# Optimization experiments

Measured on AMD Instinct MI355X. Metric: run time of the kernel, lower is better.

The kernel has to match this reference:

```python
import jax, jax.numpy as jnp
import numpy as np

B, S, N_STATE, N_HEAD = 8, 4096, 1024, 16
N_FREQ = 10000.0
H_DIM = N_STATE // N_HEAD          # 64
N_ROTS = H_DIM // 2                # 32


def setup_inputs() -> dict:
    key = jax.random.key(0)
    k1, k2, k3, k4, k5 = jax.random.split(key, 5)
    x = jax.random.normal(k1, (B, S, N_STATE), dtype=jnp.float32)
    # rotation angles (module inits to zeros; small random values exercise the math)
    thetas = jax.random.normal(k2, (N_ROTS,), dtype=jnp.float32) * 0.1
    # r_pairs.long() in torch -> integer plane indices; ensure i != j
    i = jax.random.randint(k3, (N_ROTS,), 0, H_DIM)
    off = jax.random.randint(k4, (N_ROTS,), 1, H_DIM)
    j = (i + off) % H_DIM
    r_pairs = jnp.stack([i, j], axis=-1).astype(jnp.int32)
    theta_scale = jnp.ones((1,), dtype=jnp.float32)
    # r_matrix inits to identity; add small noise so it is non-trivial
    r_matrix = jnp.eye(H_DIM, dtype=jnp.float32) + 0.01 * jax.random.normal(k5, (H_DIM, H_DIM), dtype=jnp.float32)
    inv_freq = 1.0 / (N_FREQ ** (jnp.arange(0, H_DIM, 2, dtype=jnp.float32) / H_DIM))
    return {"x": x, "thetas": thetas, "theta_scale": theta_scale,
            "r_matrix": r_matrix, "inv_freq": inv_freq,
            "r_pairs": r_pairs, "n_head": N_HEAD}


def reference(x, thetas, theta_scale, r_matrix, inv_freq, r_pairs, n_head):
    b, s, n_state = x.shape
    h_dim = n_state // n_head
    x2d = x.reshape(-1, h_dim)  # [B*S*H, h_dim]
    angles = thetas * theta_scale[0]

    # Sequential Givens plane rotations: x @ G(i,j,theta) only touches columns i, j.
    def step(carry, inp):
        theta, ij = inp
        i, j = ij[0], ij[1]
        c, sn = jnp.cos(theta), jnp.sin(theta)
        xi = carry[:, i]
        xj = carry[:, j]
        carry = carry.at[:, i].set(xi * c + xj * sn)
        carry = carry.at[:, j].set(-xi * sn + xj * c)
        return carry, None

    x2d, _ = jax.lax.scan(step, x2d, (angles, r_pairs))
    x2d = x2d @ r_matrix
    xh = x2d.reshape(b, s, n_head, h_dim)

    # RoPE-style sin/cos mix
    pos = jnp.arange(s, dtype=jnp.float32)
    sinu = pos[:, None] * inv_freq[None, :]          # [s, h_dim//2]
    sin = jnp.sin(sinu)[None, :, None, :]
    cos = jnp.cos(sinu)[None, :, None, :]
    x1, x2 = xh[..., ::2], xh[..., 1::2]
    out = jnp.concatenate([x1 * cos - x2 * sin, x1 * sin + x2 * cos], axis=-1)
    return out.reshape(b, s, n_state)
```

## Files before the change

### kernel.cpp

```cpp
#include <hip/hip_runtime.h>
#include <cstdint>
#include <cstddef>

#define S_LEN   4096
#define NROT    32
#define NGRP    8192

typedef __attribute__((ext_vector_type(8))) short  short8x;
typedef __attribute__((ext_vector_type(4))) float  floatx4;

typedef __attribute__((address_space(1))) unsigned int gu32;
typedef __attribute__((address_space(3))) unsigned int lu32;

__device__ __host__ inline unsigned short f2bf(float f) {
  union { float f; unsigned u; } c; c.f = f;
  unsigned u = c.u;
  return (unsigned short)((u + 0x7fffu + ((u >> 16) & 1u)) >> 16);
}
__device__ inline float bf2f(unsigned short h) {
  union { unsigned u; float f; } c; c.u = ((unsigned)h) << 16;
  return c.f;
}

__global__ void setup_kernel(const float* __restrict__ thetas,
                             const float* __restrict__ theta_scale,
                             const float* __restrict__ r_matrix,
                             const int*   __restrict__ r_pairs,
                             const float* __restrict__ inv_freq,
                             uint4* __restrict__ Bfrag,
                             float2* __restrict__ csT) {
  if (blockIdx.x < 512) {
    int idx = blockIdx.x * 256 + threadIdx.x;
    int s = idx >> 5;
    int f = idx & 31;
    float ang = (float)s * inv_freq[f];
    csT[idx] = make_float2(cosf(ang), sinf(ang));
    return;
  }
  __shared__ float C[64 * 65];
  __shared__ float Mm[64 * 64];
  int tid = threadIdx.x;
  if (tid < 64) {
    for (int c = 0; c < 64; ++c) C[tid * 65 + c] = (tid == c) ? 1.0f : 0.0f;
    float sc = theta_scale[0];
    for (int q = 0; q < NROT; ++q) {
      float th = thetas[q] * sc;
      float cs = cosf(th), sn = sinf(th);
      int i = r_pairs[2 * q], j = r_pairs[2 * q + 1];
      float xi = C[tid * 65 + i];
      float xj = C[tid * 65 + j];
      C[tid * 65 + i] =  xi * cs + xj * sn;
      C[tid * 65 + j] = -xi * sn + xj * cs;
    }
  }
  __syncthreads();
  for (int o = tid; o < 64 * 64; o += 256) {
    int t = o >> 6, c = o & 63;
    float a = 0.0f;
    for (int k = 0; k < 64; ++k) a = fmaf(C[t * 65 + k], r_matrix[k * 64 + c], a);
    Mm[o] = a;
  }
  __syncthreads();
  for (int e = tid; e < 16 * 64; e += 256) {
    int f = e >> 6, l = e & 63;
    int hl = f & 1, ks = (f >> 1) & 1, nt = f >> 2;
    int col = nt * 16 + (l & 15);
    unsigned short w[8];
    for (int j = 0; j < 8; ++j) {
      int k = ks * 32 + (l >> 4) * 8 + j;
      float m = Mm[k * 64 + col];
      unsigned short h = f2bf(m);
      if (hl == 0) w[j] = h;
      else         w[j] = f2bf(m - bf2f(h));
    }
    uint4 pk;
    pk.x = (unsigned)w[0] | ((unsigned)w[1] << 16);
    pk.y = (unsigned)w[2] | ((unsigned)w[3] << 16);
    pk.z = (unsigned)w[4] | ((unsigned)w[5] << 16);
    pk.w = (unsigned)w[6] | ((unsigned)w[7] << 16);
    Bfrag[e] = pk;
  }
}

__global__ __launch_bounds__(256, 3)
void rotary_main(const float* __restrict__ x,
                 const uint4* __restrict__ Bfrag,
                 const float2* __restrict__ csT,
                 float* __restrict__ out) {
  __shared__ uint4 sB[16 * 64];
  __shared__ float sobuf[4][1024];
  const int tid  = threadIdx.x;
  const int lane = tid & 63;
  const int wid  = tid >> 6;
  const int g    = blockIdx.x * 4 + wid;

  #pragma unroll
  for (int i = 0; i < 4; ++i) {
    const int chunk = i * 4 + wid;
    __builtin_amdgcn_global_load_lds(
        (gu32*)(const void*)(Bfrag + chunk * 64 + lane),
        (lu32*)(void*)(sB + chunk * 64), 16, 0, 0);
  }
  __syncthreads();

  const int lr = lane & 15;
  const int lk = lane >> 4;

  const int s0 = (g * 4) & (S_LEN - 1);
  float4 cs[4], rt[4];
  #pragma unroll
  for (int nt = 0; nt < 4; ++nt) {
    cs[nt] = *(const float4*)(csT + s0 * 32 + nt * 8 + lk * 2);
    rt[nt] = *(const float4*)(csT + 32 + nt * 8 + lk * 2);
  }
  const float* xg = x + (size_t)g * 4096;
  floatx4 a[4][4];
  #pragma unroll
  for (int t = 0; t < 4; ++t) {
    const float* xr = xg + (size_t)(t * 16 + lr) * 64 + lk * 8;
    a[t][0] = *(const floatx4*)(xr);
    a[t][1] = *(const floatx4*)(xr + 4);
    a[t][2] = *(const floatx4*)(xr + 32);
    a[t][3] = *(const floatx4*)(xr + 36);
  }
  __builtin_amdgcn_sched_barrier(0);

  float* og = out + (size_t)g * 4096;
  float* ob = &sobuf[wid][0];
  const short8x* sBf = (const short8x*)sB;
  const int okey = (lr & 7) << 2;

  #pragma unroll
  for (int t = 0; t < 4; ++t) {
    short8x Xh0, Xl0, Xh1, Xl1;
    #pragma unroll
    for (int i = 0; i < 8; ++i) {
      float v0 = (i < 4) ? a[t][0][i] : a[t][1][i - 4];
      float v1 = (i < 4) ? a[t][2][i] : a[t][3][i - 4];
      unsigned u0 = __builtin_bit_cast(unsigned, v0);
      unsigned u1 = __builtin_bit_cast(unsigned, v1);
      unsigned short h0 = (unsigned short)(u0 >> 16);
      unsigned short h1 = (unsigned short)(u1 >> 16);
      Xh0[i] = (short)h0; Xl0[i] = (short)f2bf(v0 - bf2f(h0));
      Xh1[i] = (short)h1; Xl1[i] = (short)f2bf(v1 - bf2f(h1));
    }

    #pragma unroll
    for (int nt = 0; nt < 4; ++nt) {
      short8x b0 = sBf[(nt * 4 + 0) * 64 + lane];
      short8x b1 = sBf[(nt * 4 + 1) * 64 + lane];
      short8x b2 = sBf[(nt * 4 + 2) * 64 + lane];
      short8x b3 = sBf[(nt * 4 + 3) * 64 + lane];

      floatx4 acc0 = {0.f, 0.f, 0.f, 0.f};
      floatx4 acc1 = {0.f, 0.f, 0.f, 0.f};
      acc0 = __builtin_amdgcn_mfma_f32_16x16x32_bf16(b0, Xh0, acc0, 0, 0, 0);
      acc1 = __builtin_amdgcn_mfma_f32_16x16x32_bf16(b2, Xh1, acc1, 0, 0, 0);
      acc0 = __builtin_amdgcn_mfma_f32_16x16x32_bf16(b1, Xh0, acc0, 0, 0, 0);
      acc1 = __builtin_amdgcn_mfma_f32_16x16x32_bf16(b3, Xh1, acc1, 0, 0, 0);
      acc0 = __builtin_amdgcn_mfma_f32_16x16x32_bf16(b0, Xl0, acc0, 0, 0, 0);
      acc1 = __builtin_amdgcn_mfma_f32_16x16x32_bf16(b2, Xl1, acc1, 0, 0, 0);

      const float a0 = acc0[0] + acc1[0];
      const float b0v = acc0[1] + acc1[1];
      const float a1 = acc0[2] + acc1[2];
      const float b1v = acc0[3] + acc1[3];
      float2 ev, od;
      ev.x = fmaf(a0, cs[nt].x, -(b0v * cs[nt].y));
      ev.y = fmaf(a1, cs[nt].z, -(b1v * cs[nt].w));
      od.x = fmaf(a0, cs[nt].y,   b0v * cs[nt].x);
      od.y = fmaf(a1, cs[nt].w,   b1v * cs[nt].z);
      float* ow = ob + lr * 64;
      *(float2*)(ow + ((     nt * 8 + lk * 2) ^ okey)) = ev;
      *(float2*)(ow + ((32 + nt * 8 + lk * 2) ^ okey)) = od;
    }

    if (t < 3) {
      #pragma unroll
      for (int nt = 0; nt < 4; ++nt) {
        float c0 = cs[nt].x, s0v = cs[nt].y, c1 = cs[nt].z, s1v = cs[nt].w;
        cs[nt].x = fmaf(c0, rt[nt].x, -(s0v * rt[nt].y));
        cs[nt].y = fmaf(c0, rt[nt].y,   s0v * rt[nt].x);
        cs[nt].z = fmaf(c1, rt[nt].z, -(s1v * rt[nt].w));
        cs[nt].w = fmaf(c1, rt[nt].w,   s1v * rt[nt].z);
      }
    }

    asm volatile("s_waitcnt lgkmcnt(0)" ::: "memory");
    __builtin_amdgcn_sched_barrier(0);
    #pragma unroll
    for (int q = 0; q < 4; ++q) {
      const int row = q * 4 + lk;
      const float* rp = ob + row * 64 + ((lr * 4) ^ ((row & 7) << 2));
      floatx4 vr = *(const floatx4*)rp;
      *(floatx4*)(og + (size_t)(t * 16 + row) * 64 + lr * 4) = vr;
    }
  }
}

extern "C" void kernel_launch(void* const* d_in, const int* in_sizes, int n_in,
                              void* d_out, int out_size, void* d_ws, size_t ws_size,
                              hipStream_t stream) {
  const float* x           = (const float*)d_in[0];
  const float* thetas      = (const float*)d_in[1];
  const float* theta_scale = (const float*)d_in[2];
  const float* r_matrix    = (const float*)d_in[3];
  const float* inv_freq    = (const float*)d_in[4];
  const int*   r_pairs     = (const int*)d_in[5];

  uint4*  Bfrag = (uint4*)d_ws;
  float2* csT   = (float2*)((char*)d_ws + 16384);
  float*  outp  = (float*)d_out;

  setup_kernel<<<513, 256, 0, stream>>>(thetas, theta_scale, r_matrix, r_pairs,
                                        inv_freq, Bfrag, csT);
  rotary_main<<<NGRP / 4, 256, 0, stream>>>(x, Bfrag, csT, outp);
}
```

Baseline: 77.14 us.

## Stream x tiles through a triple-buffered LDS ring with async global_load_lds

```diff
diff --git a/kernel.cpp b/kernel.cpp
--- a/kernel.cpp
+++ b/kernel.cpp
@@ -82,13 +82,13 @@
   }
 }
 
-__global__ __launch_bounds__(256, 3)
+__global__ __launch_bounds__(256)
 void rotary_main(const float* __restrict__ x,
                  const uint4* __restrict__ Bfrag,
                  const float2* __restrict__ csT,
                  float* __restrict__ out) {
+  __shared__ float sstage[4][3][1024];
   __shared__ uint4 sB[16 * 64];
-  __shared__ float sobuf[4][1024];
   const int tid  = threadIdx.x;
   const int lane = tid & 63;
   const int wid  = tid >> 6;
@@ -113,30 +113,52 @@
     cs[nt] = *(const float4*)(csT + s0 * 32 + nt * 8 + lk * 2);
     rt[nt] = *(const float4*)(csT + 32 + nt * 8 + lk * 2);
   }
+  __builtin_amdgcn_sched_barrier(0);
+
   const float* xg = x + (size_t)g * 4096;
-  floatx4 a[4][4];
+  float* og = out + (size_t)g * 4096;
+  float* stg = &sstage[wid][0][0];
+
+  #define STAGE(t, b) {                                                     \
+    float* dst_ = stg + (b) * 1024;                                         \
+    _Pragma("unroll")                                                       \
+    for (int q_ = 0; q_ < 4; ++q_) {                                        \
+      const int row_ = q_ * 4 + lk;                                         \
+      const int gs_  = lr ^ (row_ & 7);                                     \
+      __builtin_amdgcn_global_load_lds(                                     \
+        (gu32*)(const void*)(xg + (size_t)((t) * 16 + row_) * 64 + gs_ * 4),\
+        (lu32*)(void*)(dst_ + q_ * 256), 16, 0, 0);                         \
+    }                                                                       \
+  }
+
+  STAGE(0, 0)
+  STAGE(1, 1)
+  STAGE(2, 2)
+  __builtin_amdgcn_sched_barrier(0);
+
+  const short8x* sBf = (const short8x*)sB;
+  const int key  = lr & 7;
+  const int okey = key << 2;
+
   #pragma unroll
   for (int t = 0; t < 4; ++t) {
-    const float* xr = xg + (size_t)(t * 16 + lr) * 64 + lk * 8;
-    a[t][0] = *(const floatx4*)(xr);
-    a[t][1] = *(const floatx4*)(xr + 4);
-    a[t][2] = *(const floatx4*)(xr + 32);
-    a[t][3] = *(const floatx4*)(xr + 36);
-  }
-  __builtin_amdgcn_sched_barrier(0);
-
-  float* og = out + (size_t)g * 4096;
-  float* ob = &sobuf[wid][0];
-  const short8x* sBf = (const short8x*)sB;
-  const int okey = (lr & 7) << 2;
-
-  #pragma unroll
-  for (int t = 0; t < 4; ++t) {
+    if (t == 0 || t == 3) { asm volatile("s_waitcnt vmcnt(8)"  ::: "memory"); }
+    else                  { asm volatile("s_waitcnt vmcnt(12)" ::: "memory"); }
+    __builtin_amdgcn_sched_barrier(0);
+
+    float* buf = stg + (t % 3) * 1024;
+
+    const float* bb = buf + lr * 64;
+    floatx4 x0 = *(const floatx4*)(bb + (((lk * 2 + 0)    ) ^ key) * 4);
+    floatx4 x1 = *(const floatx4*)(bb + (((lk * 2 + 1)    ) ^ key) * 4);
+    floatx4 x2 = *(const floatx4*)(bb + (((lk * 2 + 0) + 8) ^ key) * 4);
+    floatx4 x3 = *(const floatx4*)(bb + (((lk * 2 + 1) + 8) ^ key) * 4);
+
     short8x Xh0, Xl0, Xh1, Xl1;
     #pragma unroll
     for (int i = 0; i < 8; ++i) {
-      float v0 = (i < 4) ? a[t][0][i] : a[t][1][i - 4];
-      float v1 = (i < 4) ? a[t][2][i] : a[t][3][i - 4];
+      float v0 = (i < 4) ? x0[i] : x1[i - 4];
+      float v1 = (i < 4) ? x2[i] : x3[i - 4];
       unsigned u0 = __builtin_bit_cast(unsigned, v0);
       unsigned u1 = __builtin_bit_cast(unsigned, v1);
       unsigned short h0 = (unsigned short)(u0 >> 16);
@@ -161,16 +183,16 @@
       acc0 = __builtin_amdgcn_mfma_f32_16x16x32_bf16(b0, Xl0, acc0, 0, 0, 0);
       acc1 = __builtin_amdgcn_mfma_f32_16x16x32_bf16(b2, Xl1, acc1, 0, 0, 0);
 
-      const float a0 = acc0[0] + acc1[0];
+      const float a0  = acc0[0] + acc1[0];
       const float b0v = acc0[1] + acc1[1];
-      const float a1 = acc0[2] + acc1[2];
+      const float a1  = acc0[2] + acc1[2];
       const float b1v = acc0[3] + acc1[3];
       float2 ev, od;
       ev.x = fmaf(a0, cs[nt].x, -(b0v * cs[nt].y));
       ev.y = fmaf(a1, cs[nt].z, -(b1v * cs[nt].w));
       od.x = fmaf(a0, cs[nt].y,   b0v * cs[nt].x);
       od.y = fmaf(a1, cs[nt].w,   b1v * cs[nt].z);
-      float* ow = ob + lr * 64;
+      float* ow = buf + lr * 64;
       *(float2*)(ow + ((     nt * 8 + lk * 2) ^ okey)) = ev;
       *(float2*)(ow + ((32 + nt * 8 + lk * 2) ^ okey)) = od;
     }
@@ -191,11 +213,18 @@
     #pragma unroll
     for (int q = 0; q < 4; ++q) {
       const int row = q * 4 + lk;
-      const float* rp = ob + row * 64 + ((lr * 4) ^ ((row & 7) << 2));
+      const float* rp = buf + row * 64 + ((lr * 4) ^ ((row & 7) << 2));
       floatx4 vr = *(const floatx4*)rp;
       *(floatx4*)(og + (size_t)(t * 16 + row) * 64 + lr * 4) = vr;
     }
-  }
+
+    if (t == 0) {
+      __builtin_amdgcn_sched_barrier(0);
+      STAGE(3, 0)
+      __builtin_amdgcn_sched_barrier(0);
+    }
+  }
+  #undef STAGE
 }
 
 extern "C" void kernel_launch(void* const* d_in, const int* in_sizes, int n_in,
```

Result: faster. 75.58 us (-2.0%).
